# Optimization experiments

Hardware: AMD Instinct MI355X
Metric: run time of the kernel (lower is better)

## Reference

```python
import jax, jax.numpy as jnp
import numpy as np

N = 20000       # num_nodes
E = 640000      # num_edges
LATENT = 64
HIDDEN = 128
NFEAT = 64
NEG_SLOPE = 0.2


def _gat_conv(x, src, dst, W, a_s, a_d, b):
    """Single-head GAT layer. x: [N, Fin]; W: [Fout, Fin]; a_s, a_d, b: [Fout]."""
    h = x @ W.T                                   # [N, Fout]
    # per-node attention logits, gathered per edge
    e = jax.nn.leaky_relu((h @ a_s)[src] + (h @ a_d)[dst], NEG_SLOPE)  # [E]
    # segment softmax over incoming edges of each target node
    m = jax.ops.segment_max(e, dst, num_segments=N)                    # [N]
    ex = jnp.exp(e - m[dst])                                           # [E]
    s = jax.ops.segment_sum(ex, dst, num_segments=N)                   # [N]
    alpha = ex / (s[dst] + 1e-16)                                      # [E]
    out = jax.ops.segment_sum(h[src] * alpha[:, None], dst, num_segments=N)  # [N, Fout]
    return out + b


def setup_inputs() -> dict:
    key = jax.random.key(0)
    ks = jax.random.split(key, 16)
    g = lambda k, shp, sc: (jax.random.normal(k, shp, dtype=jnp.float32) * sc)
    return {
        "z": g(ks[0], (LATENT,), 1.0),
        "edge_index": jax.random.randint(ks[1], (2, E), 0, N, dtype=jnp.int64 if jax.config.jax_enable_x64 else jnp.int32),
        "fc_w": g(ks[2], (N * LATENT, LATENT), 0.05),
        "fc_b": g(ks[3], (N * LATENT,), 0.05),
        "W0": g(ks[4], (HIDDEN, LATENT), 0.05),
        "as0": g(ks[5], (HIDDEN,), 0.05),
        "ad0": g(ks[6], (HIDDEN,), 0.05),
        "b0": jnp.zeros((HIDDEN,), jnp.float32),
        "W1": g(ks[7], (HIDDEN, HIDDEN), 0.05),
        "as1": g(ks[8], (HIDDEN,), 0.05),
        "ad1": g(ks[9], (HIDDEN,), 0.05),
        "b1": jnp.zeros((HIDDEN,), jnp.float32),
        "W2": g(ks[10], (NFEAT, HIDDEN), 0.05),
        "as2": g(ks[11], (NFEAT,), 0.05),
        "ad2": g(ks[12], (NFEAT,), 0.05),
        "b2": jnp.zeros((NFEAT,), jnp.float32),
    }


def reference(z, edge_index, fc_w, fc_b, W0, as0, ad0, b0, W1, as1, ad1, b1, W2, as2, ad2, b2):
    src, dst = edge_index[0], edge_index[1]
    # latent -> per-node features
    x = jax.nn.relu(z @ fc_w.T + fc_b).reshape(N, LATENT)
    x = jax.nn.relu(_gat_conv(x, src, dst, W0, as0, ad0, b0))
    x = jax.nn.relu(_gat_conv(x, src, dst, W1, as1, ad1, b1))
    x = _gat_conv(x, src, dst, W2, as2, ad2, b2)   # [N, NFEAT], no relu on last
    return x
```

## Files before the change

### kernel.cpp

```cpp
#include <hip/hip_runtime.h>
#include <hip/hip_bf16.h>

#define NEG_SLOPE 0.2f

__device__ __forceinline__ float wave_red_sum(float v) {
    for (int o = 32; o > 0; o >>= 1) v += __shfl_xor(v, o, 64);
    return v;
}
__device__ __forceinline__ float wave_red_max(float v) {
    for (int o = 32; o > 0; o >>= 1) v = fmaxf(v, __shfl_xor(v, o, 64));
    return v;
}

__global__ void fc_kernel(const float* __restrict__ z, const float* __restrict__ fcw,
                          const float* __restrict__ fcb, float* __restrict__ x, int R) {
    int t = blockIdx.x * 256 + threadIdx.x;
    int r = t >> 4;
    int j = t & 15;
    if (r >= R) return;
    float4 wz = ((const float4*)z)[j];
    float4 ww = ((const float4*)fcw)[r * 16 + j];
    float p = wz.x * ww.x + wz.y * ww.y + wz.z * ww.z + wz.w * ww.w;
    p += __shfl_xor(p, 1, 64);
    p += __shfl_xor(p, 2, 64);
    p += __shfl_xor(p, 4, 64);
    p += __shfl_xor(p, 8, 64);
    if (j == 0) {
        float v = p + fcb[r];
        x[r] = v > 0.f ? v : 0.f;
    }
}

template <int FIN, int FOUT, int NV>
__global__ void gemm_kernel(const float* __restrict__ x, const float* __restrict__ W,
                            float* __restrict__ h) {
    constexpr int KC = 64;
    constexpr int VG = 256 / FOUT;
    constexpr int NPB = VG * NV;
    __shared__ float Ws[FOUT * KC];
    __shared__ float xs[NPB * FIN];
    const int tid = threadIdx.x;
    const int f = tid % FOUT;
    const int vg = tid / FOUT;
    const int v0 = blockIdx.x * NPB;

    for (int i = tid; i < NPB * FIN; i += 256) xs[i] = x[v0 * FIN + i];

    float acc[NV];
#pragma unroll
    for (int j = 0; j < NV; j++) acc[j] = 0.f;

    for (int c0 = 0; c0 < FIN; c0 += KC) {
        __syncthreads();
        for (int i = tid; i < FOUT * KC; i += 256) {
            int ff = i / KC, kk = i % KC;
            Ws[ff * KC + ((kk + ff) & (KC - 1))] = W[ff * FIN + c0 + kk];
        }
        __syncthreads();
#pragma unroll 4
        for (int kk = 0; kk < KC; kk++) {
            float w = Ws[f * KC + ((kk + f) & (KC - 1))];
#pragma unroll
            for (int j = 0; j < NV; j++)
                acc[j] += w * xs[(vg * NV + j) * FIN + c0 + kk];
        }
    }
#pragma unroll
    for (int j = 0; j < NV; j++) {
        int v = vg * NV + j;
        h[(v0 + v) * FOUT + f] = acc[j];
    }
}

template <int FOUT>
__global__ void att_kernel(const float* __restrict__ h, const float* __restrict__ as,
                           const float* __restrict__ ad, float* __restrict__ hs,
                           float* __restrict__ hd, int N) {
    int wave = threadIdx.x >> 6;
    int lane = threadIdx.x & 63;
    int v = blockIdx.x * 4 + wave;
    if (v >= N) return;
    float ps = 0.f, pd = 0.f;
#pragma unroll
    for (int f = lane; f < FOUT; f += 64) {
        float hv = h[v * FOUT + f];
        ps += hv * as[f];
        pd += hv * ad[f];
    }
    ps = wave_red_sum(ps);
    pd = wave_red_sum(pd);
    if (lane == 0) { hs[v] = ps; hd[v] = pd; }
}

__global__ void hist_kernel(const int* __restrict__ dst, int* __restrict__ cnt, int E) {
    int e = blockIdx.x * 256 + threadIdx.x;
    if (e < E) atomicAdd(&cnt[dst[e]], 1);
}

__global__ void scan1_kernel(const int* __restrict__ cnt, int* __restrict__ rowtmp,
                             int* __restrict__ bsum) {
    __shared__ int sd[256];
    int i = blockIdx.x * 256 + threadIdx.x;
    sd[threadIdx.x] = cnt[i];
    for (int off = 1; off < 256; off <<= 1) {
        __syncthreads();
        int t = (threadIdx.x >= off) ? sd[threadIdx.x - off] : 0;
        __syncthreads();
        sd[threadIdx.x] += t;
    }
    __syncthreads();
    rowtmp[i] = sd[threadIdx.x];
    if (threadIdx.x == 255) bsum[blockIdx.x] = sd[255];
}

__global__ void scan2_kernel(const int* __restrict__ bsum, int* __restrict__ boff, int nb) {
    __shared__ int sd[128];
    int i = threadIdx.x;
    int orig = (i < nb) ? bsum[i] : 0;
    sd[i] = orig;
    for (int off = 1; off < 128; off <<= 1) {
        __syncthreads();
        int t = (i >= off) ? sd[i - off] : 0;
        __syncthreads();
        sd[i] += t;
    }
    __syncthreads();
    if (i < nb) boff[i] = sd[i] - orig;
}

__global__ void scan3_kernel(const int* __restrict__ cnt, const int* __restrict__ rowtmp,
                             const int* __restrict__ boff, int* __restrict__ rowptr,
                             int* __restrict__ cursor, int N) {
    int i = blockIdx.x * 256 + threadIdx.x;
    if (i > N) return;
    int b = i >> 8;
    int excl = boff[b] + rowtmp[i] - cnt[i];
    rowptr[i] = excl;
    if (i < N) cursor[i] = excl;
}

__global__ void scatter_kernel(const int* __restrict__ src, const int* __restrict__ dst,
                               int* __restrict__ cursor, int* __restrict__ col, int E) {
    int e = blockIdx.x * 256 + threadIdx.x;
    if (e < E) {
        int p = atomicAdd(&cursor[dst[e]], 1);
        col[p] = src[e];
    }
}

template <int FOUT, bool RELU>
__global__ void agg_kernel(const float* __restrict__ h, const float* __restrict__ hs,
                           const float* __restrict__ hd, const int* __restrict__ rowptr,
                           const int* __restrict__ col, const float* __restrict__ b,
                           float* __restrict__ out) {
    const int v = blockIdx.x;
    const int lane = threadIdx.x;
    const int s0 = rowptr[v], s1 = rowptr[v + 1];
    if (s1 == s0) {
        float bv = b[lane];
        if (RELU) bv = bv > 0.f ? bv : 0.f;
        out[v * FOUT + lane] = bv;
        if (FOUT == 128) {
            float b2 = b[lane + 64];
            if (RELU) b2 = b2 > 0.f ? b2 : 0.f;
            out[v * FOUT + 64 + lane] = b2;
        }
        return;
    }
    const float hdv = hd[v];
    float m = -1e30f;
    for (int base = s0; base < s1; base += 64) {
        int j = base + lane;
        if (j < s1) {
            float e = hs[col[j]] + hdv;
            e = e > 0.f ? e : NEG_SLOPE * e;
            m = fmaxf(m, e);
        }
    }
    m = wave_red_max(m);
    float ssum = 0.f;
    for (int base = s0; base < s1; base += 64) {
        int j = base + lane;
        if (j < s1) {
            float e = hs[col[j]] + hdv;
            e = e > 0.f ? e : NEG_SLOPE * e;
            ssum += __expf(e - m);
        }
    }
    ssum = wave_red_sum(ssum);
    float acc0 = 0.f, acc1 = 0.f;
    for (int base = s0; base < s1; base += 64) {
        int j = base + lane;
        int sv = 0;
        float w = 0.f;
        if (j < s1) {
            sv = col[j];
            float e = hs[sv] + hdv;
            e = e > 0.f ? e : NEG_SLOPE * e;
            w = __expf(e - m);
        }
        int cnt = min(64, s1 - base);
        for (int jj = 0; jj < cnt; jj++) {
            float wj = __shfl(w, jj, 64);
            int svj = __shfl(sv, jj, 64);
            acc0 += wj * h[svj * FOUT + lane];
            if (FOUT == 128) acc1 += wj * h[svj * FOUT + 64 + lane];
        }
    }
    float inv = 1.f / (ssum + 1e-16f);
    float o0 = acc0 * inv + b[lane];
    if (RELU) o0 = o0 > 0.f ? o0 : 0.f;
    out[v * FOUT + lane] = o0;
    if (FOUT == 128) {
        float o1 = acc1 * inv + b[lane + 64];
        if (RELU) o1 = o1 > 0.f ? o1 : 0.f;
        out[v * FOUT + 64 + lane] = o1;
    }
}

extern "C" void kernel_launch(void* const* d_in, const int* in_sizes, int n_in,
                              void* d_out, int out_size, void* d_ws, size_t ws_size,
                              hipStream_t stream) {
    const float* z   = (const float*)d_in[0];
    const int*   ei  = (const int*)d_in[1];
    const float* fcw = (const float*)d_in[2];
    const float* fcb = (const float*)d_in[3];
    const float* W0  = (const float*)d_in[4];
    const float* as0 = (const float*)d_in[5];
    const float* ad0 = (const float*)d_in[6];
    const float* b0  = (const float*)d_in[7];
    const float* W1  = (const float*)d_in[8];
    const float* as1 = (const float*)d_in[9];
    const float* ad1 = (const float*)d_in[10];
    const float* b1  = (const float*)d_in[11];
    const float* W2  = (const float*)d_in[12];
    const float* as2 = (const float*)d_in[13];
    const float* ad2 = (const float*)d_in[14];
    const float* b2  = (const float*)d_in[15];

    const int E = in_sizes[1] / 2;
    const int R = in_sizes[3];
    const int N = R / 64;
    const int* src = ei;
    const int* dst = ei + E;

    float* xbuf = (float*)d_ws;
    float* hbuf = xbuf + (size_t)N * 64;
    float* obuf = hbuf + (size_t)N * 128;
    float* hs   = obuf + (size_t)N * 128;
    float* hd   = hs + N;
    int* cnt    = (int*)(hd + N);
    int* rowtmp = cnt + 20480;
    int* rowptr = rowtmp + 20480;
    int* cursor = rowptr + 20032;
    int* bsum   = cursor + 20000;
    int* boff   = bsum + 128;
    int* col    = boff + 128;

    hipMemsetAsync(cnt, 0, 20480 * sizeof(int), stream);
    hist_kernel<<<(E + 255) / 256, 256, 0, stream>>>(dst, cnt, E);
    scan1_kernel<<<80, 256, 0, stream>>>(cnt, rowtmp, bsum);
    scan2_kernel<<<1, 128, 0, stream>>>(bsum, boff, 80);
    scan3_kernel<<<79, 256, 0, stream>>>(cnt, rowtmp, boff, rowptr, cursor, N);
    scatter_kernel<<<(E + 255) / 256, 256, 0, stream>>>(src, dst, cursor, col, E);

    fc_kernel<<<R / 16, 256, 0, stream>>>(z, fcw, fcb, xbuf, R);

    gemm_kernel<64, 128, 8><<<N / 16, 256, 0, stream>>>(xbuf, W0, hbuf);
    att_kernel<128><<<N / 4, 256, 0, stream>>>(hbuf, as0, ad0, hs, hd, N);
    agg_kernel<128, true><<<N, 64, 0, stream>>>(hbuf, hs, hd, rowptr, col, b0, obuf);

    gemm_kernel<128, 128, 8><<<N / 16, 256, 0, stream>>>(obuf, W1, hbuf);
    att_kernel<128><<<N / 4, 256, 0, stream>>>(hbuf, as1, ad1, hs, hd, N);
    agg_kernel<128, true><<<N, 64, 0, stream>>>(hbuf, hs, hd, rowptr, col, b1, obuf);

    gemm_kernel<128, 64, 8><<<N / 32, 256, 0, stream>>>(obuf, W2, hbuf);
    att_kernel<64><<<N / 4, 256, 0, stream>>>(hbuf, as2, ad2, hs, hd, N);
    agg_kernel<64, false><<<N, 64, 0, stream>>>(hbuf, hs, hd, rowptr, col, b2, (float*)d_out);
}
```

Baseline: 784.7 us.

## Use split-bf16 MFMA GEMM fused with attention, and a 4-wave cached-weight aggregation

Replaces the FP32 shared-memory GEMM with bf16 MFMA (16x16x32) and uses a hi/lo bf16 split with three products to keep near-FP32 accuracy. The per-node attention dot products are folded into the GEMM epilogue, which removes the separate att kernels. The aggregation kernel now runs 4 nodes per 256-thread block and caches edge weights and source indices in LDS, so logits are computed once instead of three times. Its output is written directly as split bf16 for the next layer. This adds a weight-split kernel and extra MFMA work, and the bf16 split may carry small precision error.

After: 670.0 us. -14.6%, faster.

```diff
diff --git a/kernel.cpp b/kernel.cpp
--- a/kernel.cpp
+++ b/kernel.cpp
@@ -1,7 +1,9 @@
 #include <hip/hip_runtime.h>
-#include <hip/hip_bf16.h>
 
 #define NEG_SLOPE 0.2f
+
+typedef __attribute__((ext_vector_type(8))) short short8;
+typedef __attribute__((ext_vector_type(4))) float v4f;
 
 __device__ __forceinline__ float wave_red_sum(float v) {
     for (int o = 32; o > 0; o >>= 1) v += __shfl_xor(v, o, 64);
@@ -11,9 +13,23 @@
     for (int o = 32; o > 0; o >>= 1) v = fmaxf(v, __shfl_xor(v, o, 64));
     return v;
 }
+__device__ __forceinline__ unsigned short f2bf(float f) {
+    union { float f; unsigned int u; } x; x.f = f;
+    unsigned int r = x.u + 0x7fffu + ((x.u >> 16) & 1u);
+    return (unsigned short)(r >> 16);
+}
+__device__ __forceinline__ float bf2f(unsigned short b) {
+    union { unsigned int u; float f; } x; x.u = ((unsigned int)b) << 16;
+    return x.f;
+}
+__device__ __forceinline__ void split_bf(float v, unsigned short& hi, unsigned short& lo) {
+    hi = f2bf(v);
+    lo = f2bf(v - bf2f(hi));
+}
 
 __global__ void fc_kernel(const float* __restrict__ z, const float* __restrict__ fcw,
-                          const float* __restrict__ fcb, float* __restrict__ x, int R) {
+                          const float* __restrict__ fcb, unsigned short* __restrict__ xhi,
+                          unsigned short* __restrict__ xlo, int R) {
     int t = blockIdx.x * 256 + threadIdx.x;
     int r = t >> 4;
     int j = t & 15;
@@ -27,69 +43,93 @@
     p += __shfl_xor(p, 8, 64);
     if (j == 0) {
         float v = p + fcb[r];
-        x[r] = v > 0.f ? v : 0.f;
-    }
-}
-
-template <int FIN, int FOUT, int NV>
-__global__ void gemm_kernel(const float* __restrict__ x, const float* __restrict__ W,
-                            float* __restrict__ h) {
-    constexpr int KC = 64;
-    constexpr int VG = 256 / FOUT;
-    constexpr int NPB = VG * NV;
-    __shared__ float Ws[FOUT * KC];
-    __shared__ float xs[NPB * FIN];
-    const int tid = threadIdx.x;
-    const int f = tid % FOUT;
-    const int vg = tid / FOUT;
-    const int v0 = blockIdx.x * NPB;
-
-    for (int i = tid; i < NPB * FIN; i += 256) xs[i] = x[v0 * FIN + i];
-
-    float acc[NV];
-#pragma unroll
-    for (int j = 0; j < NV; j++) acc[j] = 0.f;
-
-    for (int c0 = 0; c0 < FIN; c0 += KC) {
-        __syncthreads();
-        for (int i = tid; i < FOUT * KC; i += 256) {
-            int ff = i / KC, kk = i % KC;
-            Ws[ff * KC + ((kk + ff) & (KC - 1))] = W[ff * FIN + c0 + kk];
-        }
-        __syncthreads();
-#pragma unroll 4
-        for (int kk = 0; kk < KC; kk++) {
-            float w = Ws[f * KC + ((kk + f) & (KC - 1))];
-#pragma unroll
-            for (int j = 0; j < NV; j++)
-                acc[j] += w * xs[(vg * NV + j) * FIN + c0 + kk];
-        }
-    }
-#pragma unroll
-    for (int j = 0; j < NV; j++) {
-        int v = vg * NV + j;
-        h[(v0 + v) * FOUT + f] = acc[j];
-    }
-}
-
-template <int FOUT>
-__global__ void att_kernel(const float* __restrict__ h, const float* __restrict__ as,
-                           const float* __restrict__ ad, float* __restrict__ hs,
-                           float* __restrict__ hd, int N) {
-    int wave = threadIdx.x >> 6;
-    int lane = threadIdx.x & 63;
-    int v = blockIdx.x * 4 + wave;
-    if (v >= N) return;
-    float ps = 0.f, pd = 0.f;
-#pragma unroll
-    for (int f = lane; f < FOUT; f += 64) {
-        float hv = h[v * FOUT + f];
-        ps += hv * as[f];
-        pd += hv * ad[f];
-    }
-    ps = wave_red_sum(ps);
-    pd = wave_red_sum(pd);
-    if (lane == 0) { hs[v] = ps; hd[v] = pd; }
+        v = v > 0.f ? v : 0.f;
+        unsigned short hi, lo;
+        split_bf(v, hi, lo);
+        xhi[r] = hi;
+        xlo[r] = lo;
+    }
+}
+
+__global__ void wsplit_kernel(const float* __restrict__ W0, const float* __restrict__ W1,
+                              const float* __restrict__ W2, int n0, int n1, int n2,
+                              unsigned short* __restrict__ whi, unsigned short* __restrict__ wlo) {
+    int i = blockIdx.x * 256 + threadIdx.x;
+    if (i >= n0 + n1 + n2) return;
+    float v;
+    if (i < n0) v = W0[i];
+    else if (i < n0 + n1) v = W1[i - n0];
+    else v = W2[i - n0 - n1];
+    unsigned short hi, lo;
+    split_bf(v, hi, lo);
+    whi[i] = hi;
+    wlo[i] = lo;
+}
+
+template <int FIN, int FOUT>
+__global__ __launch_bounds__(256) void gemm_att_kernel(
+        const unsigned short* __restrict__ xhi, const unsigned short* __restrict__ xlo,
+        const unsigned short* __restrict__ whi, const unsigned short* __restrict__ wlo,
+        const float* __restrict__ as, const float* __restrict__ ad,
+        float* __restrict__ h, float* __restrict__ hs, float* __restrict__ hd, int Mtiles) {
+    constexpr int NT = FOUT / 16;
+    constexpr int KS = FIN / 32;
+    const int wid = blockIdx.x * 4 + (threadIdx.x >> 6);
+    if (wid >= Mtiles) return;
+    const int lane = threadIdx.x & 63;
+    const int l15 = lane & 15;
+    const int quad = lane >> 4;
+    const int v0 = wid * 16;
+
+    v4f acc[NT];
+#pragma unroll
+    for (int nt = 0; nt < NT; nt++) acc[nt] = (v4f){0.f, 0.f, 0.f, 0.f};
+
+    const unsigned short* xh = xhi + (v0 + l15) * FIN + quad * 8;
+    const unsigned short* xl = xlo + (v0 + l15) * FIN + quad * 8;
+    const unsigned short* wh = whi + l15 * FIN + quad * 8;
+    const unsigned short* wl = wlo + l15 * FIN + quad * 8;
+#pragma unroll
+    for (int ks = 0; ks < KS; ks++) {
+        short8 ah = *(const short8*)(xh + ks * 32);
+        short8 al = *(const short8*)(xl + ks * 32);
+#pragma unroll
+        for (int nt = 0; nt < NT; nt++) {
+            short8 bh = *(const short8*)(wh + nt * 16 * FIN + ks * 32);
+            short8 bl = *(const short8*)(wl + nt * 16 * FIN + ks * 32);
+            acc[nt] = __builtin_amdgcn_mfma_f32_16x16x32_bf16(ah, bh, acc[nt], 0, 0, 0);
+            acc[nt] = __builtin_amdgcn_mfma_f32_16x16x32_bf16(ah, bl, acc[nt], 0, 0, 0);
+            acc[nt] = __builtin_amdgcn_mfma_f32_16x16x32_bf16(al, bh, acc[nt], 0, 0, 0);
+        }
+    }
+    float ps[4] = {0.f, 0.f, 0.f, 0.f}, pd[4] = {0.f, 0.f, 0.f, 0.f};
+#pragma unroll
+    for (int nt = 0; nt < NT; nt++) {
+        float av = as[nt * 16 + l15];
+        float dv = ad[nt * 16 + l15];
+#pragma unroll
+        for (int r = 0; r < 4; r++) {
+            float c = acc[nt][r];
+            h[(v0 + quad * 4 + r) * FOUT + nt * 16 + l15] = c;
+            ps[r] += c * av;
+            pd[r] += c * dv;
+        }
+    }
+#pragma unroll
+    for (int o = 8; o >= 1; o >>= 1) {
+#pragma unroll
+        for (int r = 0; r < 4; r++) {
+            ps[r] += __shfl_xor(ps[r], o, 64);
+            pd[r] += __shfl_xor(pd[r], o, 64);
+        }
+    }
+    if (l15 == 0) {
+#pragma unroll
+        for (int r = 0; r < 4; r++) {
+            hs[v0 + quad * 4 + r] = ps[r];
+            hd[v0 + quad * 4 + r] = pd[r];
+        }
+    }
 }
 
 __global__ void hist_kernel(const int* __restrict__ dst, int* __restrict__ cnt, int E) {
@@ -148,73 +188,105 @@
     }
 }
 
-template <int FOUT, bool RELU>
-__global__ void agg_kernel(const float* __restrict__ h, const float* __restrict__ hs,
-                           const float* __restrict__ hd, const int* __restrict__ rowptr,
-                           const int* __restrict__ col, const float* __restrict__ b,
-                           float* __restrict__ out) {
-    const int v = blockIdx.x;
-    const int lane = threadIdx.x;
-    const int s0 = rowptr[v], s1 = rowptr[v + 1];
-    if (s1 == s0) {
-        float bv = b[lane];
-        if (RELU) bv = bv > 0.f ? bv : 0.f;
-        out[v * FOUT + lane] = bv;
-        if (FOUT == 128) {
-            float b2 = b[lane + 64];
-            if (RELU) b2 = b2 > 0.f ? b2 : 0.f;
-            out[v * FOUT + 64 + lane] = b2;
-        }
-        return;
-    }
-    const float hdv = hd[v];
-    float m = -1e30f;
-    for (int base = s0; base < s1; base += 64) {
-        int j = base + lane;
-        if (j < s1) {
-            float e = hs[col[j]] + hdv;
-            e = e > 0.f ? e : NEG_SLOPE * e;
-            m = fmaxf(m, e);
-        }
-    }
-    m = wave_red_max(m);
-    float ssum = 0.f;
-    for (int base = s0; base < s1; base += 64) {
-        int j = base + lane;
-        if (j < s1) {
-            float e = hs[col[j]] + hdv;
-            e = e > 0.f ? e : NEG_SLOPE * e;
-            ssum += __expf(e - m);
-        }
-    }
-    ssum = wave_red_sum(ssum);
-    float acc0 = 0.f, acc1 = 0.f;
-    for (int base = s0; base < s1; base += 64) {
-        int j = base + lane;
-        int sv = 0;
-        float w = 0.f;
-        if (j < s1) {
-            sv = col[j];
+template <int FOUT, bool RELU, bool SPLIT>
+__global__ __launch_bounds__(256) void agg_kernel(
+        const float* __restrict__ h, const float* __restrict__ hs, const float* __restrict__ hd,
+        const int* __restrict__ rowptr, const int* __restrict__ col, const float* __restrict__ b,
+        float* __restrict__ out, unsigned short* __restrict__ ohi,
+        unsigned short* __restrict__ olo) {
+    constexpr int FPT = FOUT / 64;
+    constexpr int CAP = 512;
+    __shared__ float sw[4][CAP];
+    __shared__ int ssv[4][CAP];
+    const int w = threadIdx.x >> 6;
+    const int lane = threadIdx.x & 63;
+    const int v = blockIdx.x * 4 + w;
+    float* swv = sw[w];
+    int* ssvv = ssv[w];
+    const int s0 = rowptr[v];
+    const int deg = rowptr[v + 1] - s0;
+    float acc[FPT];
+#pragma unroll
+    for (int i = 0; i < FPT; i++) acc[i] = 0.f;
+    float inv = 0.f;
+    if (deg > 0) {
+        const float hdv = hd[v];
+        float mt = -1e30f;
+        for (int j = lane; j < deg; j += 64) {
+            int sv = col[s0 + j];
             float e = hs[sv] + hdv;
             e = e > 0.f ? e : NEG_SLOPE * e;
-            w = __expf(e - m);
-        }
-        int cnt = min(64, s1 - base);
-        for (int jj = 0; jj < cnt; jj++) {
-            float wj = __shfl(w, jj, 64);
-            int svj = __shfl(sv, jj, 64);
-            acc0 += wj * h[svj * FOUT + lane];
-            if (FOUT == 128) acc1 += wj * h[svj * FOUT + 64 + lane];
-        }
-    }
-    float inv = 1.f / (ssum + 1e-16f);
-    float o0 = acc0 * inv + b[lane];
-    if (RELU) o0 = o0 > 0.f ? o0 : 0.f;
-    out[v * FOUT + lane] = o0;
-    if (FOUT == 128) {
-        float o1 = acc1 * inv + b[lane + 64];
-        if (RELU) o1 = o1 > 0.f ? o1 : 0.f;
-        out[v * FOUT + 64 + lane] = o1;
+            if (j < CAP) { ssvv[j] = sv; swv[j] = e; }
+            mt = fmaxf(mt, e);
+        }
+        const float m = wave_red_max(mt);
+        float st = 0.f;
+        for (int j = lane; j < deg; j += 64) {
+            float e;
+            if (j < CAP) e = swv[j];
+            else {
+                int sv = col[s0 + j];
+                e = hs[sv] + hdv;
+                e = e > 0.f ? e : NEG_SLOPE * e;
+            }
+            float ww = __expf(e - m);
+            if (j < CAP) swv[j] = ww;
+            st += ww;
+        }
+        const float ssum = wave_red_sum(st);
+        inv = 1.f / (ssum + 1e-16f);
+        const int dmain = deg < CAP ? deg : CAP;
+#pragma unroll 4
+        for (int jj = 0; jj < dmain; jj++) {
+            float ww = swv[jj];
+            int sv = ssvv[jj];
+            if (FPT == 2) {
+                float2 hv = ((const float2*)(h + sv * FOUT))[lane];
+                acc[0] += ww * hv.x;
+                acc[1] += ww * hv.y;
+            } else {
+                acc[0] += ww * h[sv * FOUT + lane];
+            }
+        }
+        for (int jj = CAP; jj < deg; jj++) {
+            int sv = col[s0 + jj];
+            float e = hs[sv] + hdv;
+            e = e > 0.f ? e : NEG_SLOPE * e;
+            float ww = __expf(e - m);
+            if (FPT == 2) {
+                float2 hv = ((const float2*)(h + sv * FOUT))[lane];
+                acc[0] += ww * hv.x;
+                acc[1] += ww * hv.y;
+            } else {
+                acc[0] += ww * h[sv * FOUT + lane];
+            }
+        }
+    }
+    float o[FPT];
+#pragma unroll
+    for (int i = 0; i < FPT; i++) {
+        float bv = b[lane * FPT + i];
+        o[i] = acc[i] * inv + bv;
+        if (RELU) o[i] = fmaxf(o[i], 0.f);
+    }
+    if (SPLIT) {
+        if (FPT == 2) {
+            unsigned short h0, l0, h1, l1;
+            split_bf(o[0], h0, l0);
+            split_bf(o[1], h1, l1);
+            ((ushort2*)ohi)[v * 64 + lane] = make_ushort2(h0, h1);
+            ((ushort2*)olo)[v * 64 + lane] = make_ushort2(l0, l1);
+        } else {
+            unsigned short hb, lb;
+            split_bf(o[0], hb, lb);
+            ohi[v * FOUT + lane] = hb;
+            olo[v * FOUT + lane] = lb;
+        }
+    } else {
+        if (FPT == 2)
+            ((float2*)out)[v * 64 + lane] = make_float2(o[0], o[1]);
+        else
+            out[v * FOUT + lane] = o[0];
     }
 }
 
@@ -241,40 +313,57 @@
     const int E = in_sizes[1] / 2;
     const int R = in_sizes[3];
     const int N = R / 64;
+    const int n0 = in_sizes[4];
+    const int n1 = in_sizes[8];
+    const int n2 = in_sizes[12];
     const int* src = ei;
     const int* dst = ei + E;
 
-    float* xbuf = (float*)d_ws;
-    float* hbuf = xbuf + (size_t)N * 64;
-    float* obuf = hbuf + (size_t)N * 128;
-    float* hs   = obuf + (size_t)N * 128;
-    float* hd   = hs + N;
-    int* cnt    = (int*)(hd + N);
-    int* rowtmp = cnt + 20480;
-    int* rowptr = rowtmp + 20480;
-    int* cursor = rowptr + 20032;
-    int* bsum   = cursor + 20000;
-    int* boff   = bsum + 128;
-    int* col    = boff + 128;
-
-    hipMemsetAsync(cnt, 0, 20480 * sizeof(int), stream);
+    char* p = (char*)d_ws;
+    auto carve = [&](size_t bytes) {
+        void* r = (void*)p;
+        p += (bytes + 255) & ~(size_t)255;
+        return r;
+    };
+    unsigned short* xhi = (unsigned short*)carve((size_t)N * 128 * 2);
+    unsigned short* xlo = (unsigned short*)carve((size_t)N * 128 * 2);
+    float* hbuf = (float*)carve((size_t)N * 128 * 4);
+    float* hs = (float*)carve((size_t)N * 4);
+    float* hd = (float*)carve((size_t)N * 4);
+    unsigned short* whi = (unsigned short*)carve((size_t)(n0 + n1 + n2) * 2);
+    unsigned short* wlo = (unsigned short*)carve((size_t)(n0 + n1 + n2) * 2);
+    const int nb = (N + 255) / 256;
+    int* cnt = (int*)carve((size_t)nb * 256 * 4);
+    int* rowtmp = (int*)carve((size_t)nb * 256 * 4);
+    int* rowptr = (int*)carve((size_t)(N + 32) * 4);
+    int* cursor = (int*)carve((size_t)N * 4);
+    int* bsum = (int*)carve(128 * 4);
+    int* boff = (int*)carve(128 * 4);
+    int* col = (int*)carve((size_t)E * 4);
+
+    hipMemsetAsync(cnt, 0, (size_t)nb * 256 * 4, stream);
     hist_kernel<<<(E + 255) / 256, 256, 0, stream>>>(dst, cnt, E);
-    scan1_kernel<<<80, 256, 0, stream>>>(cnt, rowtmp, bsum);
-    scan2_kernel<<<1, 128, 0, stream>>>(bsum, boff, 80);
-    scan3_kernel<<<79, 256, 0, stream>>>(cnt, rowtmp, boff, rowptr, cursor, N);
+    scan1_kernel<<<nb, 256, 0, stream>>>(cnt, rowtmp, bsum);
+    scan2_kernel<<<1, 128, 0, stream>>>(bsum, boff, nb);
+    scan3_kernel<<<(N + 256) / 256, 256, 0, stream>>>(cnt, rowtmp, boff, rowptr, cursor, N);
     scatter_kernel<<<(E + 255) / 256, 256, 0, stream>>>(src, dst, cursor, col, E);
 
-    fc_kernel<<<R / 16, 256, 0, stream>>>(z, fcw, fcb, xbuf, R);
-
-    gemm_kernel<64, 128, 8><<<N / 16, 256, 0, stream>>>(xbuf, W0, hbuf);
-    att_kernel<128><<<N / 4, 256, 0, stream>>>(hbuf, as0, ad0, hs, hd, N);
-    agg_kernel<128, true><<<N, 64, 0, stream>>>(hbuf, hs, hd, rowptr, col, b0, obuf);
-
-    gemm_kernel<128, 128, 8><<<N / 16, 256, 0, stream>>>(obuf, W1, hbuf);
-    att_kernel<128><<<N / 4, 256, 0, stream>>>(hbuf, as1, ad1, hs, hd, N);
-    agg_kernel<128, true><<<N, 64, 0, stream>>>(hbuf, hs, hd, rowptr, col, b1, obuf);
-
-    gemm_kernel<128, 64, 8><<<N / 32, 256, 0, stream>>>(obuf, W2, hbuf);
-    att_kernel<64><<<N / 4, 256, 0, stream>>>(hbuf, as2, ad2, hs, hd, N);
-    agg_kernel<64, false><<<N, 64, 0, stream>>>(hbuf, hs, hd, rowptr, col, b2, (float*)d_out);
-}
+    wsplit_kernel<<<(n0 + n1 + n2 + 255) / 256, 256, 0, stream>>>(W0, W1, W2, n0, n1, n2, whi, wlo);
+    fc_kernel<<<R / 16, 256, 0, stream>>>(z, fcw, fcb, xhi, xlo, R);
+
+    const int Mtiles = N / 16;
+    const int gblocks = (Mtiles + 3) / 4;
+
+    gemm_att_kernel<64, 128><<<gblocks, 256, 0, stream>>>(xhi, xlo, whi, wlo, as0, ad0,
+                                                          hbuf, hs, hd, Mtiles);
+    agg_kernel<128, true, true><<<N / 4, 256, 0, stream>>>(hbuf, hs, hd, rowptr, col, b0,
+                                                           nullptr, xhi, xlo);
+    gemm_att_kernel<128, 128><<<gblocks, 256, 0, stream>>>(xhi, xlo, whi + n0, wlo + n0, as1, ad1,
+                                                           hbuf, hs, hd, Mtiles);
+    agg_kernel<128, true, true><<<N / 4, 256, 0, stream>>>(hbuf, hs, hd, rowptr, col, b1,
+                                                           nullptr, xhi, xlo);
+    gemm_att_kernel<128, 64><<<gblocks, 256, 0, stream>>>(xhi, xlo, whi + n0 + n1, wlo + n0 + n1,
+                                                          as2, ad2, hbuf, hs, hd, Mtiles);
+    agg_kernel<64, false, false><<<N / 4, 256, 0, stream>>>(hbuf, hs, hd, rowptr, col, b2,
+                                                            (float*)d_out, nullptr, nullptr);
+}
```
